# Optimization experiments

Hardware: AMD Instinct MI355X
Metric: run time of the kernel (lower is better)

## Reference

```python
import jax, jax.numpy as jnp
import numpy as np

UNITS = 128
INPUT_DIM = 784
OUTPUT_DIM = 10
NUM_LAYERS = 8
BATCH = 2048
DT = 0.1
EPS = 0.01
TOL = 1e-4
STEPS = 15


def setup_inputs() -> dict:
    key = jax.random.key(0)
    k = jax.random.split(key, 7)
    s_in = 1.0 / np.sqrt(INPUT_DIM)
    s_u = 1.0 / np.sqrt(UNITS)
    return {
        "x": jax.random.normal(k[0], (BATCH, INPUT_DIM), jnp.float32),
        "w_in": jax.random.uniform(k[1], (UNITS, INPUT_DIM), jnp.float32, -s_in, s_in),
        "b_in": jax.random.uniform(k[2], (UNITS,), jnp.float32, -s_in, s_in),
        "w_blocks": jax.random.uniform(k[3], (NUM_LAYERS, UNITS, UNITS), jnp.float32, -s_u, s_u),
        "b_blocks": jax.random.uniform(k[4], (NUM_LAYERS, UNITS), jnp.float32, -s_u, s_u),
        "w_out": jax.random.uniform(k[5], (OUTPUT_DIM, UNITS), jnp.float32, -s_u, s_u),
        "b_out": jax.random.uniform(k[6], (OUTPUT_DIM,), jnp.float32, -s_u, s_u),
    }


def _build_A(w_blocks):
    # A_l = [[I, dt*W_l], [-dt*W_l^T, (1+dt/eps)*I]], shape [L, 2u, 2u]
    I = jnp.broadcast_to(jnp.eye(UNITS, dtype=w_blocks.dtype), (NUM_LAYERS, UNITS, UNITS))
    top = jnp.concatenate([I, DT * w_blocks], axis=2)
    bot = jnp.concatenate([-DT * jnp.transpose(w_blocks, (0, 2, 1)), (1.0 + DT / EPS) * I], axis=2)
    return jnp.concatenate([top, bot], axis=1)


def _sweep(z_in, A, b_blocks):
    # Fixed-point sweeping (no-grad region in the original). z_ls: [L, B, 2u]
    B = z_in.shape[0]

    def layer_step(z, xs):
        A_l, b_l, z_l = xs
        rhs = jnp.concatenate(
            [jnp.broadcast_to(DT * b_l, (B, UNITS)), (DT / EPS) * jnp.tanh(z_l[:, :UNITS])],
            axis=1,
        ) + z
        # A_l is shared across the batch: one LU, many rhs
        y = jnp.linalg.solve(A_l, rhs.T).T
        err = jnp.mean(jnp.linalg.norm(z_l - y, axis=1))
        return y, (y, err)

    def body(state):
        z_ls, _, step = state
        _, (new_zls, errs) = jax.lax.scan(layer_step, z_in, (A, b_blocks, z_ls))
        return (new_zls, jnp.mean(errs), step + 1)

    def cond(state):
        _, err, step = state
        return jnp.logical_and(step < STEPS, err > TOL)

    z0 = jnp.broadcast_to(z_in[None], (NUM_LAYERS,) + z_in.shape)
    z_ls, _, _ = jax.lax.while_loop(cond, body, (z0, jnp.float32(10.0), jnp.int32(0)))
    return z_ls


def _block(z_in, W, b, z_l):
    # implicit_forward of one TransNetLayerSweeping (z_l is the converged sweep state)
    u_l, v_l = z_l[:, :UNITS], z_l[:, UNITS:]
    u_out = -DT * (v_l @ W.T) + z_in[:, :UNITS] + DT * b
    v_out = DT * (u_l @ W) + z_in[:, UNITS:] - (DT / EPS) * (v_l - jnp.tanh(u_l))
    return jnp.concatenate([u_out, v_out], axis=1)


def reference(x, w_in, b_in, w_blocks, b_blocks, w_out, b_out):
    x1 = x @ w_in.T + b_in                                  # [B, u]
    z_in = jnp.concatenate([x1, jnp.tanh(x1)], axis=1)      # [B, 2u]
    z_ls = _sweep(z_in, _build_A(w_blocks), b_blocks)       # [L, B, 2u]
    # Original loop does z = block.implicit_forward(z_in) for every block,
    # so only the LAST block's output survives.
    z_out = _block(z_in, w_blocks[-1], b_blocks[-1], z_ls[-1])
    logits = z_out[:, :UNITS] @ w_out.T + b_out             # [B, out]
    return jax.nn.softmax(logits, axis=1)
```

## Files before the change

kernel.cpp:

```cpp
#include <hip/hip_runtime.h>

#define U 128
#define BATCH 2048
#define NL 8
#define NS 8
#define DTc 0.1f
#define TENf 10.0f
#define INVC (1.0f/11.0f)
#define AFACT (0.01f/11.0f)
#define AST 264

typedef unsigned short u16;
typedef __attribute__((ext_vector_type(8))) short bf16x8;
typedef __attribute__((ext_vector_type(4))) float f32x4;
#define MFMA16(a,b,c) __builtin_amdgcn_mfma_f32_16x16x32_bf16(a,b,c,0,0,0)

__device__ __forceinline__ float bf2f(u16 h){ return __uint_as_float(((unsigned int)h)<<16); }
__device__ __forceinline__ u16 f2bf(float f){
  unsigned int u = __float_as_uint(f);
  u += 0x7FFFu + ((u >> 16) & 1u);
  return (u16)(u >> 16);
}
__device__ __forceinline__ float fast_tanh(float x){
  float e = __expf(2.0f*x);
  return 1.0f - __fdividef(2.0f, e + 1.0f);
}
__device__ __forceinline__ int detect_md(const u16* x, int* s_bad, int t, int nthr){
  if(t==0) *s_bad = 0;
  __syncthreads();
  int f=0;
  for(int i=t;i<4096;i+=nthr){ float v = bf2f(x[i]); if(!(fabsf(v)<16.0f)) f=1; }
  if(f) atomicOr(s_bad,1);
  __syncthreads();
  return *s_bad ? 0 : 1;
}

__global__ __launch_bounds__(256) void convK(
    const void* __restrict__ xraw, const void* __restrict__ w_in,
    const void* __restrict__ b_in, const void* __restrict__ wb,
    const void* __restrict__ bb, const void* __restrict__ w_out,
    const void* __restrict__ b_out,
    u16* __restrict__ winb, u16* __restrict__ Wg, u16* __restrict__ Wtg,
    float* __restrict__ bbD, float* __restrict__ b_in_f,
    float* __restrict__ w_out_f, float* __restrict__ b_out_f){
  __shared__ int s_bad;
  const int t = threadIdx.x;
  const int md = detect_md((const u16*)xraw, &s_bad, t, 256);
  const int g = blockIdx.x*256 + t, GS = gridDim.x*256;
  for(int i=g;i<100352;i+=GS) winb[i] = md ? ((const u16*)w_in)[i] : f2bf(((const float*)w_in)[i]);
  for(int i=g;i<131072;i+=GS){
    u16 h = md ? ((const u16*)wb)[i] : f2bf(((const float*)wb)[i]);
    Wg[i] = h;
    int L = i>>14, j = i & 16383;
    Wtg[(L<<14) + (j&127)*U + (j>>7)] = h;
  }
  for(int i=g;i<NL*U;i+=GS) bbD[i] = DTc * (md ? bf2f(((const u16*)bb)[i]) : ((const float*)bb)[i]);
  for(int i=g;i<U;i+=GS)    b_in_f[i]  = md ? bf2f(((const u16*)b_in)[i])  : ((const float*)b_in)[i];
  for(int i=g;i<1280;i+=GS) w_out_f[i] = md ? bf2f(((const u16*)w_out)[i]) : ((const float*)w_out)[i];
  for(int i=g;i<10;i+=GS)   b_out_f[i] = md ? bf2f(((const u16*)b_out)[i]) : ((const float*)b_out)[i];
}

template<typename EPI>
__device__ __forceinline__ void tile16(const u16* __restrict__ A, int lda,
                                       const u16* __restrict__ B, int ldb, EPI epi){
  const int lane = threadIdx.x & 63, w = threadIdx.x >> 6;
  const int ln = lane & 15, lq = lane >> 4;
  const int n0 = 32*w + ln, n1 = n0 + 16;
  bf16x8 af[4], b0[4], b1[4];
  #pragma unroll
  for(int kt=0;kt<4;kt++){
    af[kt] = *(const bf16x8*)&A[ln*lda + kt*32 + lq*8];
    b0[kt] = *(const bf16x8*)&B[n0*ldb + kt*32 + lq*8];
    b1[kt] = *(const bf16x8*)&B[n1*ldb + kt*32 + lq*8];
  }
  f32x4 a0 = {0,0,0,0}, a1 = {0,0,0,0};
  #pragma unroll
  for(int kt=0;kt<4;kt++){ a0 = MFMA16(af[kt], b0[kt], a0); a1 = MFMA16(af[kt], b1[kt], a1); }
  epi(a0, a1, n0, n1);
}

__global__ __launch_bounds__(256) void gemmP(const u16* __restrict__ Wtg, u16* __restrict__ Pg){
  const int L = blockIdx.x >> 3, mt = blockIdx.x & 7;
  const int lq = (threadIdx.x & 63) >> 4;
  const u16* WtL = Wtg + (L<<14);
  tile16(WtL + mt*16*U, U, WtL, U, [&](f32x4 a0, f32x4 a1, int n0, int n1){
    #pragma unroll
    for(int r=0;r<4;r++){
      int row = mt*16 + lq*4 + r;
      Pg[(L<<14) + row*U + n0] = f2bf(AFACT*a0[r]);
      Pg[(L<<14) + row*U + n1] = f2bf(AFACT*a1[r]);
    }
  });
}
__global__ __launch_bounds__(256) void gemmS(const u16* __restrict__ Pg, u16* __restrict__ Fb){
  const int L = blockIdx.x >> 3, mt = blockIdx.x & 7;
  const int lq = (threadIdx.x & 63) >> 4;
  const u16* PL = Pg + (L<<14);
  u16* FbL = Fb + (size_t)L*65536;
  tile16(PL + mt*16*U, U, PL, U, [&](f32x4 a0, f32x4 a1, int n0, int n1){
    #pragma unroll
    for(int r=0;r<4;r++){
      int row = mt*16 + lq*4 + r;
      FbL[row*256 + n0] = f2bf(INVC*(((row==n0)?1.0f:0.0f) - bf2f(PL[row*U+n0]) + a0[r]));
      FbL[row*256 + n1] = f2bf(INVC*(((row==n1)?1.0f:0.0f) - bf2f(PL[row*U+n1]) + a1[r]));
    }
  });
}
__global__ __launch_bounds__(256) void gemmQ(const u16* __restrict__ Fb, const u16* __restrict__ Wg,
                                             u16* __restrict__ FbW){
  const int L = blockIdx.x >> 3, mt = blockIdx.x & 7;
  const int lq = (threadIdx.x & 63) >> 4;
  const u16* FbL = Fb + (size_t)L*65536;
  u16* FbO = FbW + (size_t)L*65536;
  tile16(FbL + mt*16*256, 256, Wg + (L<<14), U, [&](f32x4 a0, f32x4 a1, int n0, int n1){
    #pragma unroll
    for(int r=0;r<4;r++){
      int row = mt*16 + lq*4 + r;
      u16 q0 = f2bf(DTc*a0[r]), q1 = f2bf(DTc*a1[r]);
      FbO[row*256 + 128 + n0] = q0;
      FbO[row*256 + 128 + n1] = q1;
      FbO[(128+n0)*256 + row] = q0;
      FbO[(128+n1)*256 + row] = q1;
    }
  });
}
__global__ __launch_bounds__(256) void gemmR(const u16* __restrict__ Wg, u16* __restrict__ Fb){
  const int L = blockIdx.x >> 3, mt = blockIdx.x & 7;
  const int lq = (threadIdx.x & 63) >> 4;
  u16* FbL = Fb + (size_t)L*65536;
  tile16(Wg + (L<<14) + mt*16*U, U, FbL + 128*256, 256, [&](f32x4 a0, f32x4 a1, int n0, int n1){
    #pragma unroll
    for(int r=0;r<4;r++){
      int row = mt*16 + lq*4 + r;
      FbL[(128+row)*256 + 128 + n0] = f2bf(DTc*a0[r]);
      FbL[(128+row)*256 + 128 + n1] = f2bf(DTc*a1[r]);
    }
  });
}
__global__ __launch_bounds__(256) void swizK(const u16* __restrict__ Fb, u16* __restrict__ Fsw){
  const int L = blockIdx.x >> 3, part = blockIdx.x & 7;
  const u16* FbL = Fb + (size_t)L*65536;
  for(int i = part*1024 + threadIdx.x; i < (part+1)*1024; i += 256){
    int lanei = i & 63, kt = (i>>6)&7, c = (i>>9)&3, w = (i>>11)&3;
    int lni = lanei & 15, lqi = lanei >> 4;
    int row_n = 64*w + 16*c + lni;
    int col_k = kt*32 + lqi*8;
    *(bf16x8*)&Fsw[((size_t)L*8192 + i)*8] = *(const bf16x8*)&FbL[row_n*256 + col_k];
  }
}

__global__ __launch_bounds__(512,1) void mainK(
    const void* __restrict__ xraw, const u16* __restrict__ winb,
    const float* __restrict__ b_in_f, const bf16x8* __restrict__ Fsw,
    const float* __restrict__ bbD, const float* __restrict__ w_out_f,
    const float* __restrict__ b_out_f, void* __restrict__ outraw){
  __shared__ u16 At[2][16*AST];
  __shared__ unsigned zh32[NL][16][64];
  __shared__ float zinu[16*U];
  __shared__ float bbL[NL*U];
  __shared__ float lg[16*12];
  __shared__ int s_bad;
  float* uout = (float*)&At[0][0];

  const int t = threadIdx.x;
  const int lane = t & 63, wid = t >> 6, ln = lane & 15, lq = lane >> 4;
  const int r0 = blockIdx.x * 16;

  const int md = detect_md((const u16*)xraw, &s_bad, t, 512);
  for(int i=t;i<NL*U;i+=512) bbL[i] = bbD[i];
  __syncthreads();

  {
    const int n0 = 16*wid + ln;
    f32x4 acc = {0,0,0,0};
    for(int kt=0; kt<25; ++kt){
      int k0 = kt*32 + lq*8;
      bf16x8 av = {0,0,0,0,0,0,0,0}, bv = {0,0,0,0,0,0,0,0};
      if(k0 < 784){
        if(md){
          av = *(const bf16x8*)((const u16*)xraw + (size_t)(r0+ln)*784 + k0);
        } else {
          const float* xp = (const float*)xraw + (size_t)(r0+ln)*784 + k0;
          float4 f0 = *(const float4*)xp, f1 = *(const float4*)(xp+4);
          av[0]=(short)f2bf(f0.x); av[1]=(short)f2bf(f0.y); av[2]=(short)f2bf(f0.z); av[3]=(short)f2bf(f0.w);
          av[4]=(short)f2bf(f1.x); av[5]=(short)f2bf(f1.y); av[6]=(short)f2bf(f1.z); av[7]=(short)f2bf(f1.w);
        }
        bv = *(const bf16x8*)&winb[(size_t)n0*784 + k0];
      }
      acc = MFMA16(av, bv, acc);
    }
    #pragma unroll
    for(int r=0;r<4;r++) zinu[(lq*4+r)*U + n0] = acc[r] + b_in_f[n0];
  }
  __syncthreads();

  for(int i=t; i<NL*16*64; i+=512){
    int l = i>>10, row = (i>>6)&15, p = i & 63;
    int lo = 32*(p>>4) + (p&15);
    zh32[l][row][p] = ((unsigned)f2bf(zinu[row*U + lo + 16]) << 16) | f2bf(zinu[row*U + lo]);
  }
  float ru[2][4];
  if(wid < 4){
    #pragma unroll
    for(int cc=0;cc<2;cc++){
      int n = 32*wid + 16*cc + ln;
      #pragma unroll
      for(int r=0;r<4;r++){
        int row = lq*4 + r;
        At[0][row*AST + n] = f2bf((TENf + 1.0f) * fast_tanh(zinu[row*U + n]));
      }
    }
  } else {
    int w4 = wid - 4;
    #pragma unroll
    for(int cc=0;cc<2;cc++){
      int uc = 32*w4 + 16*cc + ln;
      #pragma unroll
      for(int r=0;r<4;r++){
        int row = lq*4 + r;
        float v = zinu[row*U + uc] + bbL[uc];
        ru[cc][r] = v;
        At[0][row*AST + 128 + uc] = f2bf(v);
      }
    }
  }
  const bf16x8* fbase = Fsw + (wid>>1)*2048 + (wid&1)*1024 + lane;
  bf16x8 BfA[2][8], BfB[2][8];
  #pragma unroll
  for(int cc=0;cc<2;cc++){
    #pragma unroll
    for(int kt=0;kt<8;kt++) BfA[cc][kt] = fbase[cc*512 + kt*64];
  }
  __syncthreads();

#define STEPBODY(STEPV, BC, BN, CURC) { \
    const int l = (STEPV) & 7; \
    const int lnext = (l+1) & 7; \
    const bool last = ((STEPV) == NS*NL-1); \
    { const bf16x8* fp = fbase + lnext*8192; \
      _Pragma("unroll") \
      for(int cc=0;cc<2;cc++){ _Pragma("unroll") for(int kt=0;kt<8;kt++) BN[cc][kt] = fp[cc*512 + kt*64]; } } \
    bf16x8 at8[8]; \
    _Pragma("unroll") \
    for(int kt=0;kt<8;kt++) at8[kt] = *(const bf16x8*)&At[CURC][ln*AST + kt*32 + lq*8]; \
    float th[2][4]; \
    if(wid < 4 && !last){ \
      _Pragma("unroll") \
      for(int r=0;r<4;r++){ \
        unsigned pk = zh32[lnext][lq*4 + r][16*wid + ln]; \
        th[0][r] = TENf * fast_tanh(bf2f((u16)(pk & 0xffff))); \
        th[1][r] = TENf * fast_tanh(bf2f((u16)(pk >> 16))); \
      } \
    } \
    f32x4 acc[2] = {{0,0,0,0},{0,0,0,0}}; \
    _Pragma("unroll") \
    for(int kt=0;kt<8;kt++){ \
      acc[0] = MFMA16(at8[kt], BC[0][kt], acc[0]); \
      acc[1] = MFMA16(at8[kt], BC[1][kt], acc[1]); \
    } \
    if(wid < 4){ \
      if(!last){ \
        const bool wrap = (l == 7); \
        _Pragma("unroll") \
        for(int cc=0;cc<2;cc++){ \
          int n = 32*wid + 16*cc + ln; \
          _Pragma("unroll") \
          for(int r=0;r<4;r++){ \
            int row = lq*4 + r; \
            float base = wrap ? fast_tanh(zinu[row*U + n]) : acc[cc][r]; \
            At[1-(CURC)][row*AST + n] = f2bf(th[cc][r] + base); \
          } \
        } \
      } \
    } else { \
      int w4 = wid - 4; \
      _Pragma("unroll") \
      for(int r=0;r<4;r++){ \
        int row = lq*4 + r; \
        int uc0 = 32*w4 + ln; \
        float yu0 = ru[0][r] - acc[0][r]; \
        float yu1 = ru[1][r] - acc[1][r]; \
        zh32[l][row][16*w4 + ln] = ((unsigned)f2bf(yu1)<<16) | f2bf(yu0); \
        if(last){ \
          uout[row*U + uc0]      = zinu[row*U + uc0]      + bbL[7*U + uc0]      - acc[0][r]; \
          uout[row*U + uc0 + 16] = zinu[row*U + uc0 + 16] + bbL[7*U + uc0 + 16] - acc[1][r]; \
        } else if(l == 7){ \
          float rn0 = zinu[row*U + uc0]      + bbL[uc0]; \
          float rn1 = zinu[row*U + uc0 + 16] + bbL[uc0 + 16]; \
          ru[0][r] = rn0; ru[1][r] = rn1; \
          At[1-(CURC)][row*AST + 128 + uc0]      = f2bf(rn0); \
          At[1-(CURC)][row*AST + 128 + uc0 + 16] = f2bf(rn1); \
        } else { \
          float rn0 = yu0 + bbL[(l+1)*U + uc0]; \
          float rn1 = yu1 + bbL[(l+1)*U + uc0 + 16]; \
          ru[0][r] = rn0; ru[1][r] = rn1; \
          At[1-(CURC)][row*AST + 128 + uc0]      = f2bf(rn0); \
          At[1-(CURC)][row*AST + 128 + uc0 + 16] = f2bf(rn1); \
        } \
      } \
    } \
    __syncthreads(); \
  }

  for(int sp=0; sp<NS*NL; sp+=2){
    STEPBODY(sp,   BfA, BfB, 0)
    STEPBODY(sp+1, BfB, BfA, 1)
  }
#undef STEPBODY

  if(t < 160){
    int mm = t/10, o = t - mm*10;
    float a = b_out_f[o];
    const float* wo = w_out_f + o*U;
    for(int k=0;k<U;k++) a += uout[mm*U + k]*wo[k];
    lg[mm*12 + o] = a;
  }
  __syncthreads();
  if(t < 16){
    float mx = -1e30f;
    for(int o=0;o<10;o++) mx = fmaxf(mx, lg[t*12 + o]);
    float e[10]; float sum = 0.0f;
    for(int o=0;o<10;o++){ e[o] = __expf(lg[t*12 + o] - mx); sum += e[o]; }
    float inv = 1.0f / sum;
    for(int o=0;o<10;o++){
      float pv = e[o]*inv;
      if(md) ((u16*)outraw)[(size_t)(r0 + t)*10 + o] = f2bf(pv);
      else   ((float*)outraw)[(size_t)(r0 + t)*10 + o] = pv;
    }
  }
}

extern "C" void kernel_launch(void* const* d_in, const int* in_sizes, int n_in,
                              void* d_out, int out_size, void* d_ws, size_t ws_size,
                              hipStream_t stream) {
  char* p = (char*)d_ws;
  u16* Fb      = (u16*)p;  p += (size_t)8*256*256*2;
  u16* Fsw     = (u16*)p;  p += (size_t)8*256*256*2;
  u16* Wg      = (u16*)p;  p += (size_t)8*128*128*2;
  u16* Wtg     = (u16*)p;  p += (size_t)8*128*128*2;
  u16* Pg      = (u16*)p;  p += (size_t)8*128*128*2;
  u16* winb    = (u16*)p;  p += 200704;
  float* bbD   = (float*)p; p += 4096;
  float* b_in_f = (float*)p; p += 512;
  float* w_out_f = (float*)p; p += 5120;
  float* b_out_f = (float*)p; p += 64;

  convK<<<128, 256, 0, stream>>>(d_in[0], d_in[1], d_in[2], d_in[3], d_in[4],
                                 d_in[5], d_in[6],
                                 winb, Wg, Wtg, bbD, b_in_f, w_out_f, b_out_f);
  gemmP<<<64, 256, 0, stream>>>(Wtg, Pg);
  gemmS<<<64, 256, 0, stream>>>(Pg, Fb);
  gemmQ<<<64, 256, 0, stream>>>(Fb, Wg, Fb);
  gemmR<<<64, 256, 0, stream>>>(Wg, Fb);
  swizK<<<64, 256, 0, stream>>>(Fb, Fsw);
  mainK<<<BATCH/16, 512, 0, stream>>>(d_in[0], winb, b_in_f, (const bf16x8*)Fsw, bbD,
                                      w_out_f, b_out_f, d_out);
}
```

Before: 206.7 us.

## Fuse setup kernels with grid barriers and widen main kernel to 1024 threads

The six setup kernels (weight conversion, four small GEMMs, swizzle) are merged into one persistent 64-block kernel. Its stages are separated by atomic-counter grid barriers, and a tiny kernel zeroes the counters first. This removes five launch gaps. The main sweep kernel goes from 8 to 16 waves per block, with each wave owning one 16-column MFMA tile instead of two, to cut per-wave serial MFMA latency in the dependent step chain. The risks are spin-wait overhead in the grid barriers, which assume all 64 blocks are co-resident, and higher register and scheduling pressure at 1024 threads.

```diff
diff --git a/kernel.cpp b/kernel.cpp
--- a/kernel.cpp
+++ b/kernel.cpp
@@ -9,6 +9,7 @@
 #define INVC (1.0f/11.0f)
 #define AFACT (0.01f/11.0f)
 #define AST 264
+#define ZST 132
 
 typedef unsigned short u16;
 typedef __attribute__((ext_vector_type(8))) short bf16x8;
@@ -35,30 +36,18 @@
   return *s_bad ? 0 : 1;
 }
 
-__global__ __launch_bounds__(256) void convK(
-    const void* __restrict__ xraw, const void* __restrict__ w_in,
-    const void* __restrict__ b_in, const void* __restrict__ wb,
-    const void* __restrict__ bb, const void* __restrict__ w_out,
-    const void* __restrict__ b_out,
-    u16* __restrict__ winb, u16* __restrict__ Wg, u16* __restrict__ Wtg,
-    float* __restrict__ bbD, float* __restrict__ b_in_f,
-    float* __restrict__ w_out_f, float* __restrict__ b_out_f){
-  __shared__ int s_bad;
-  const int t = threadIdx.x;
-  const int md = detect_md((const u16*)xraw, &s_bad, t, 256);
-  const int g = blockIdx.x*256 + t, GS = gridDim.x*256;
-  for(int i=g;i<100352;i+=GS) winb[i] = md ? ((const u16*)w_in)[i] : f2bf(((const float*)w_in)[i]);
-  for(int i=g;i<131072;i+=GS){
-    u16 h = md ? ((const u16*)wb)[i] : f2bf(((const float*)wb)[i]);
-    Wg[i] = h;
-    int L = i>>14, j = i & 16383;
-    Wtg[(L<<14) + (j&127)*U + (j>>7)] = h;
-  }
-  for(int i=g;i<NL*U;i+=GS) bbD[i] = DTc * (md ? bf2f(((const u16*)bb)[i]) : ((const float*)bb)[i]);
-  for(int i=g;i<U;i+=GS)    b_in_f[i]  = md ? bf2f(((const u16*)b_in)[i])  : ((const float*)b_in)[i];
-  for(int i=g;i<1280;i+=GS) w_out_f[i] = md ? bf2f(((const u16*)w_out)[i]) : ((const float*)w_out)[i];
-  for(int i=g;i<10;i+=GS)   b_out_f[i] = md ? bf2f(((const u16*)b_out)[i]) : ((const float*)b_out)[i];
-}
+__device__ __forceinline__ void gbar(int* c, int idx){
+  __syncthreads();
+  if(threadIdx.x==0){
+    __threadfence();
+    atomicAdd(&c[idx], 1);
+    while(atomicAdd(&c[idx], 0) < 64){ __builtin_amdgcn_s_sleep(8); }
+    __threadfence();
+  }
+  __syncthreads();
+}
+
+__global__ void zeroK(int* g){ if(threadIdx.x < 8) g[threadIdx.x] = 0; }
 
 template<typename EPI>
 __device__ __forceinline__ void tile16(const u16* __restrict__ A, int lda,
@@ -79,55 +68,76 @@
   epi(a0, a1, n0, n1);
 }
 
-__global__ __launch_bounds__(256) void gemmP(const u16* __restrict__ Wtg, u16* __restrict__ Pg){
+__global__ __launch_bounds__(256) void setupF(
+    const void* __restrict__ xraw, const void* __restrict__ w_in,
+    const void* __restrict__ b_in, const void* __restrict__ wb,
+    const void* __restrict__ bb, const void* __restrict__ w_out,
+    const void* __restrict__ b_out,
+    u16* __restrict__ Fb, u16* __restrict__ Fsw,
+    u16* __restrict__ Wg, u16* __restrict__ Wtg,
+    u16* __restrict__ Pg, u16* __restrict__ winb,
+    float* __restrict__ bbD, float* __restrict__ b_in_f,
+    float* __restrict__ w_out_f, float* __restrict__ b_out_f,
+    int* __restrict__ gctr){
+  __shared__ int s_bad;
+  const int t = threadIdx.x;
+  const int md = detect_md((const u16*)xraw, &s_bad, t, 256);
   const int L = blockIdx.x >> 3, mt = blockIdx.x & 7;
   const int lq = (threadIdx.x & 63) >> 4;
+
+  {
+    const int g = blockIdx.x*256 + t, GS = 64*256;
+    for(int i=g;i<100352;i+=GS) winb[i] = md ? ((const u16*)w_in)[i] : f2bf(((const float*)w_in)[i]);
+    for(int i=g;i<131072;i+=GS){
+      u16 h = md ? ((const u16*)wb)[i] : f2bf(((const float*)wb)[i]);
+      Wg[i] = h;
+      int Li = i>>14, j = i & 16383;
+      Wtg[(Li<<14) + (j&127)*U + (j>>7)] = h;
+    }
+    for(int i=g;i<NL*U;i+=GS) bbD[i] = DTc * (md ? bf2f(((const u16*)bb)[i]) : ((const float*)bb)[i]);
+    for(int i=g;i<U;i+=GS)    b_in_f[i]  = md ? bf2f(((const u16*)b_in)[i])  : ((const float*)b_in)[i];
+    for(int i=g;i<1280;i+=GS) w_out_f[i] = md ? bf2f(((const u16*)w_out)[i]) : ((const float*)w_out)[i];
+    for(int i=g;i<10;i+=GS)   b_out_f[i] = md ? bf2f(((const u16*)b_out)[i]) : ((const float*)b_out)[i];
+  }
+  gbar(gctr, 0);
+
   const u16* WtL = Wtg + (L<<14);
+  u16* PgL = Pg + (L<<14);
+  u16* FbL = Fb + (size_t)L*65536;
+
   tile16(WtL + mt*16*U, U, WtL, U, [&](f32x4 a0, f32x4 a1, int n0, int n1){
     #pragma unroll
     for(int r=0;r<4;r++){
       int row = mt*16 + lq*4 + r;
-      Pg[(L<<14) + row*U + n0] = f2bf(AFACT*a0[r]);
-      Pg[(L<<14) + row*U + n1] = f2bf(AFACT*a1[r]);
+      PgL[row*U + n0] = f2bf(AFACT*a0[r]);
+      PgL[row*U + n1] = f2bf(AFACT*a1[r]);
     }
   });
-}
-__global__ __launch_bounds__(256) void gemmS(const u16* __restrict__ Pg, u16* __restrict__ Fb){
-  const int L = blockIdx.x >> 3, mt = blockIdx.x & 7;
-  const int lq = (threadIdx.x & 63) >> 4;
-  const u16* PL = Pg + (L<<14);
-  u16* FbL = Fb + (size_t)L*65536;
-  tile16(PL + mt*16*U, U, PL, U, [&](f32x4 a0, f32x4 a1, int n0, int n1){
+  gbar(gctr, 1);
+
+  tile16(PgL + mt*16*U, U, PgL, U, [&](f32x4 a0, f32x4 a1, int n0, int n1){
     #pragma unroll
     for(int r=0;r<4;r++){
       int row = mt*16 + lq*4 + r;
-      FbL[row*256 + n0] = f2bf(INVC*(((row==n0)?1.0f:0.0f) - bf2f(PL[row*U+n0]) + a0[r]));
-      FbL[row*256 + n1] = f2bf(INVC*(((row==n1)?1.0f:0.0f) - bf2f(PL[row*U+n1]) + a1[r]));
+      FbL[row*256 + n0] = f2bf(INVC*(((row==n0)?1.0f:0.0f) - bf2f(PgL[row*U+n0]) + a0[r]));
+      FbL[row*256 + n1] = f2bf(INVC*(((row==n1)?1.0f:0.0f) - bf2f(PgL[row*U+n1]) + a1[r]));
     }
   });
-}
-__global__ __launch_bounds__(256) void gemmQ(const u16* __restrict__ Fb, const u16* __restrict__ Wg,
-                                             u16* __restrict__ FbW){
-  const int L = blockIdx.x >> 3, mt = blockIdx.x & 7;
-  const int lq = (threadIdx.x & 63) >> 4;
-  const u16* FbL = Fb + (size_t)L*65536;
-  u16* FbO = FbW + (size_t)L*65536;
+  gbar(gctr, 2);
+
   tile16(FbL + mt*16*256, 256, Wg + (L<<14), U, [&](f32x4 a0, f32x4 a1, int n0, int n1){
     #pragma unroll
     for(int r=0;r<4;r++){
       int row = mt*16 + lq*4 + r;
       u16 q0 = f2bf(DTc*a0[r]), q1 = f2bf(DTc*a1[r]);
-      FbO[row*256 + 128 + n0] = q0;
-      FbO[row*256 + 128 + n1] = q1;
-      FbO[(128+n0)*256 + row] = q0;
-      FbO[(128+n1)*256 + row] = q1;
+      FbL[row*256 + 128 + n0] = q0;
+      FbL[row*256 + 128 + n1] = q1;
+      FbL[(128+n0)*256 + row] = q0;
+      FbL[(128+n1)*256 + row] = q1;
     }
   });
-}
-__global__ __launch_bounds__(256) void gemmR(const u16* __restrict__ Wg, u16* __restrict__ Fb){
-  const int L = blockIdx.x >> 3, mt = blockIdx.x & 7;
-  const int lq = (threadIdx.x & 63) >> 4;
-  u16* FbL = Fb + (size_t)L*65536;
+  gbar(gctr, 3);
+
   tile16(Wg + (L<<14) + mt*16*U, U, FbL + 128*256, 256, [&](f32x4 a0, f32x4 a1, int n0, int n1){
     #pragma unroll
     for(int r=0;r<4;r++){
@@ -136,26 +146,22 @@
       FbL[(128+row)*256 + 128 + n1] = f2bf(DTc*a1[r]);
     }
   });
-}
-__global__ __launch_bounds__(256) void swizK(const u16* __restrict__ Fb, u16* __restrict__ Fsw){
-  const int L = blockIdx.x >> 3, part = blockIdx.x & 7;
-  const u16* FbL = Fb + (size_t)L*65536;
-  for(int i = part*1024 + threadIdx.x; i < (part+1)*1024; i += 256){
-    int lanei = i & 63, kt = (i>>6)&7, c = (i>>9)&3, w = (i>>11)&3;
+  gbar(gctr, 4);
+
+  for(int i = mt*1024 + t; i < (mt+1)*1024; i += 256){
+    int lanei = i & 63, kt = (i>>6)&7, w = (i>>9)&15;
     int lni = lanei & 15, lqi = lanei >> 4;
-    int row_n = 64*w + 16*c + lni;
-    int col_k = kt*32 + lqi*8;
-    *(bf16x8*)&Fsw[((size_t)L*8192 + i)*8] = *(const bf16x8*)&FbL[row_n*256 + col_k];
-  }
-}
-
-__global__ __launch_bounds__(512,1) void mainK(
+    *(bf16x8*)&Fsw[((size_t)L*8192 + i)*8] = *(const bf16x8*)&FbL[(16*w+lni)*256 + kt*32 + lqi*8];
+  }
+}
+
+__global__ __launch_bounds__(1024) void mainK(
     const void* __restrict__ xraw, const u16* __restrict__ winb,
     const float* __restrict__ b_in_f, const bf16x8* __restrict__ Fsw,
     const float* __restrict__ bbD, const float* __restrict__ w_out_f,
     const float* __restrict__ b_out_f, void* __restrict__ outraw){
   __shared__ u16 At[2][16*AST];
-  __shared__ unsigned zh32[NL][16][64];
+  __shared__ u16 zh16[NL*16*ZST];
   __shared__ float zinu[16*U];
   __shared__ float bbL[NL*U];
   __shared__ float lg[16*12];
@@ -166,11 +172,11 @@
   const int lane = t & 63, wid = t >> 6, ln = lane & 15, lq = lane >> 4;
   const int r0 = blockIdx.x * 16;
 
-  const int md = detect_md((const u16*)xraw, &s_bad, t, 512);
-  for(int i=t;i<NL*U;i+=512) bbL[i] = bbD[i];
-  __syncthreads();
-
-  {
+  const int md = detect_md((const u16*)xraw, &s_bad, t, 1024);
+  for(int i=t;i<NL*U;i+=1024) bbL[i] = bbD[i];
+  __syncthreads();
+
+  if(wid < 8){
     const int n0 = 16*wid + ln;
     f32x4 acc = {0,0,0,0};
     for(int kt=0; kt<25; ++kt){
@@ -194,43 +200,32 @@
   }
   __syncthreads();
 
-  for(int i=t; i<NL*16*64; i+=512){
-    int l = i>>10, row = (i>>6)&15, p = i & 63;
-    int lo = 32*(p>>4) + (p&15);
-    zh32[l][row][p] = ((unsigned)f2bf(zinu[row*U + lo + 16]) << 16) | f2bf(zinu[row*U + lo]);
-  }
-  float ru[2][4];
-  if(wid < 4){
-    #pragma unroll
-    for(int cc=0;cc<2;cc++){
-      int n = 32*wid + 16*cc + ln;
-      #pragma unroll
-      for(int r=0;r<4;r++){
-        int row = lq*4 + r;
-        At[0][row*AST + n] = f2bf((TENf + 1.0f) * fast_tanh(zinu[row*U + n]));
-      }
+  for(int i=t; i<NL*16*U; i+=1024){
+    int l = i>>11, row = (i>>7)&15, c = i&127;
+    zh16[(l*16+row)*ZST + c] = f2bf(zinu[row*U + c]);
+  }
+  float ru[4];
+  if(wid < 8){
+    const int n = 16*wid + ln;
+    #pragma unroll
+    for(int r=0;r<4;r++){
+      int row = lq*4 + r;
+      At[0][row*AST + n] = f2bf((TENf + 1.0f) * fast_tanh(zinu[row*U + n]));
     }
   } else {
-    int w4 = wid - 4;
-    #pragma unroll
-    for(int cc=0;cc<2;cc++){
-      int uc = 32*w4 + 16*cc + ln;
-      #pragma unroll
-      for(int r=0;r<4;r++){
-        int row = lq*4 + r;
-        float v = zinu[row*U + uc] + bbL[uc];
-        ru[cc][r] = v;
-        At[0][row*AST + 128 + uc] = f2bf(v);
-      }
-    }
-  }
-  const bf16x8* fbase = Fsw + (wid>>1)*2048 + (wid&1)*1024 + lane;
-  bf16x8 BfA[2][8], BfB[2][8];
+    const int uc = 16*(wid-8) + ln;
+    #pragma unroll
+    for(int r=0;r<4;r++){
+      int row = lq*4 + r;
+      float v = zinu[row*U + uc] + bbL[uc];
+      ru[r] = v;
+      At[0][row*AST + 128 + uc] = f2bf(v);
+    }
+  }
+  const bf16x8* fbase = Fsw + wid*512 + lane;
+  bf16x8 BfA[8], BfB[8];
   #pragma unroll
-  for(int cc=0;cc<2;cc++){
-    #pragma unroll
-    for(int kt=0;kt<8;kt++) BfA[cc][kt] = fbase[cc*512 + kt*64];
-  }
+  for(int kt=0;kt<8;kt++) BfA[kt] = fbase[kt*64];
   __syncthreads();
 
 #define STEPBODY(STEPV, BC, BN, CURC) { \
@@ -239,63 +234,47 @@
     const bool last = ((STEPV) == NS*NL-1); \
     { const bf16x8* fp = fbase + lnext*8192; \
       _Pragma("unroll") \
-      for(int cc=0;cc<2;cc++){ _Pragma("unroll") for(int kt=0;kt<8;kt++) BN[cc][kt] = fp[cc*512 + kt*64]; } } \
+      for(int kt=0;kt<8;kt++) BN[kt] = fp[kt*64]; } \
     bf16x8 at8[8]; \
     _Pragma("unroll") \
     for(int kt=0;kt<8;kt++) at8[kt] = *(const bf16x8*)&At[CURC][ln*AST + kt*32 + lq*8]; \
-    float th[2][4]; \
-    if(wid < 4 && !last){ \
+    float th[4]; \
+    if(wid < 8 && !last){ \
       _Pragma("unroll") \
-      for(int r=0;r<4;r++){ \
-        unsigned pk = zh32[lnext][lq*4 + r][16*wid + ln]; \
-        th[0][r] = TENf * fast_tanh(bf2f((u16)(pk & 0xffff))); \
-        th[1][r] = TENf * fast_tanh(bf2f((u16)(pk >> 16))); \
-      } \
+      for(int r=0;r<4;r++) \
+        th[r] = TENf * fast_tanh(bf2f(zh16[(lnext*16 + lq*4 + r)*ZST + 16*wid + ln])); \
     } \
-    f32x4 acc[2] = {{0,0,0,0},{0,0,0,0}}; \
+    f32x4 acc = {0,0,0,0}; \
     _Pragma("unroll") \
-    for(int kt=0;kt<8;kt++){ \
-      acc[0] = MFMA16(at8[kt], BC[0][kt], acc[0]); \
-      acc[1] = MFMA16(at8[kt], BC[1][kt], acc[1]); \
-    } \
-    if(wid < 4){ \
+    for(int kt=0;kt<8;kt++) acc = MFMA16(at8[kt], BC[kt], acc); \
+    if(wid < 8){ \
       if(!last){ \
         const bool wrap = (l == 7); \
+        const int n = 16*wid + ln; \
         _Pragma("unroll") \
-        for(int cc=0;cc<2;cc++){ \
-          int n = 32*wid + 16*cc + ln; \
-          _Pragma("unroll") \
-          for(int r=0;r<4;r++){ \
-            int row = lq*4 + r; \
-            float base = wrap ? fast_tanh(zinu[row*U + n]) : acc[cc][r]; \
-            At[1-(CURC)][row*AST + n] = f2bf(th[cc][r] + base); \
-          } \
+        for(int r=0;r<4;r++){ \
+          int row = lq*4 + r; \
+          float base = wrap ? fast_tanh(zinu[row*U + n]) : acc[r]; \
+          At[1-(CURC)][row*AST + n] = f2bf(th[r] + base); \
         } \
       } \
     } else { \
-      int w4 = wid - 4; \
+      const int uc = 16*(wid-8) + ln; \
       _Pragma("unroll") \
       for(int r=0;r<4;r++){ \
         int row = lq*4 + r; \
-        int uc0 = 32*w4 + ln; \
-        float yu0 = ru[0][r] - acc[0][r]; \
-        float yu1 = ru[1][r] - acc[1][r]; \
-        zh32[l][row][16*w4 + ln] = ((unsigned)f2bf(yu1)<<16) | f2bf(yu0); \
+        float yu = ru[r] - acc[r]; \
+        zh16[(l*16+row)*ZST + uc] = f2bf(yu); \
         if(last){ \
-          uout[row*U + uc0]      = zinu[row*U + uc0]      + bbL[7*U + uc0]      - acc[0][r]; \
-          uout[row*U + uc0 + 16] = zinu[row*U + uc0 + 16] + bbL[7*U + uc0 + 16] - acc[1][r]; \
+          uout[row*U + uc] = zinu[row*U + uc] + bbL[7*U + uc] - acc[r]; \
         } else if(l == 7){ \
-          float rn0 = zinu[row*U + uc0]      + bbL[uc0]; \
-          float rn1 = zinu[row*U + uc0 + 16] + bbL[uc0 + 16]; \
-          ru[0][r] = rn0; ru[1][r] = rn1; \
-          At[1-(CURC)][row*AST + 128 + uc0]      = f2bf(rn0); \
-          At[1-(CURC)][row*AST + 128 + uc0 + 16] = f2bf(rn1); \
+          float rn = zinu[row*U + uc] + bbL[uc]; \
+          ru[r] = rn; \
+          At[1-(CURC)][row*AST + 128 + uc] = f2bf(rn); \
         } else { \
-          float rn0 = yu0 + bbL[(l+1)*U + uc0]; \
-          float rn1 = yu1 + bbL[(l+1)*U + uc0 + 16]; \
-          ru[0][r] = rn0; ru[1][r] = rn1; \
-          At[1-(CURC)][row*AST + 128 + uc0]      = f2bf(rn0); \
-          At[1-(CURC)][row*AST + 128 + uc0 + 16] = f2bf(rn1); \
+          float rn = yu + bbL[(l+1)*U + uc]; \
+          ru[r] = rn; \
+          At[1-(CURC)][row*AST + 128 + uc] = f2bf(rn); \
         } \
       } \
     } \
@@ -344,15 +323,13 @@
   float* b_in_f = (float*)p; p += 512;
   float* w_out_f = (float*)p; p += 5120;
   float* b_out_f = (float*)p; p += 64;
-
-  convK<<<128, 256, 0, stream>>>(d_in[0], d_in[1], d_in[2], d_in[3], d_in[4],
+  int* gctr    = (int*)p;  p += 64;
+
+  zeroK<<<1, 64, 0, stream>>>(gctr);
+  setupF<<<64, 256, 0, stream>>>(d_in[0], d_in[1], d_in[2], d_in[3], d_in[4],
                                  d_in[5], d_in[6],
-                                 winb, Wg, Wtg, bbD, b_in_f, w_out_f, b_out_f);
-  gemmP<<<64, 256, 0, stream>>>(Wtg, Pg);
-  gemmS<<<64, 256, 0, stream>>>(Pg, Fb);
-  gemmQ<<<64, 256, 0, stream>>>(Fb, Wg, Fb);
-  gemmR<<<64, 256, 0, stream>>>(Wg, Fb);
-  swizK<<<64, 256, 0, stream>>>(Fb, Fsw);
-  mainK<<<BATCH/16, 512, 0, stream>>>(d_in[0], winb, b_in_f, (const bf16x8*)Fsw, bbD,
-                                      w_out_f, b_out_f, d_out);
-}
+                                 Fb, Fsw, Wg, Wtg, Pg, winb, bbD, b_in_f,
+                                 w_out_f, b_out_f, gctr);
+  mainK<<<BATCH/16, 1024, 0, stream>>>(d_in[0], winb, b_in_f, (const bf16x8*)Fsw, bbD,
+                                       w_out_f, b_out_f, d_out);
+}
```

Result: slower. 235.4 us (+13.9%).
